# Optimization experiments

Measured on AMD Instinct MI355X. Metric: run time of the kernel, lower is better.

## Reference

```python
import jax, jax.numpy as jnp
import numpy as np

B, NP, K, E = 8, 4096, 1024, 262144   # graphs, nodes/graph, topk keep, edges
N = B * NP
EPS = 1e-5


def _glorot(k, fi, fo):
    lim = float(np.sqrt(6.0 / (fi + fo)))
    return jax.random.uniform(k, (fi, fo), jnp.float32, -lim, lim)


def setup_inputs() -> dict:
    key = jax.random.key(0)
    ks = jax.random.split(key, 16)
    pos = jax.random.normal(ks[0], (N, 3), jnp.float32)
    epg = E // B
    src = jax.random.randint(ks[1], (E,), 0, NP)
    dst = jax.random.randint(ks[2], (E,), 0, NP)
    off = jnp.repeat(jnp.arange(B) * NP, epg)   # edges stay within their graph
    edge_index = jnp.stack([src + off, dst + off]).astype(jnp.int32)
    batch = jnp.repeat(jnp.arange(B, dtype=jnp.int32), NP)
    inp = {"pos": pos, "edge_index": edge_index, "batch": batch,
           "p": jax.random.normal(ks[3], (3,), jnp.float32)}
    dims = [3, 64, 128, 128, 256, 512]
    for i in range(5):
        fi, fo = dims[i], dims[i + 1]
        inp[f"W{i+1}"] = _glorot(ks[4 + i], fi, fo)
        inp[f"b{i+1}"] = jnp.zeros((fo,), jnp.float32)
        inp[f"g{i+1}"] = jnp.ones((fo,), jnp.float32)
        inp[f"be{i+1}"] = jnp.zeros((fo,), jnp.float32)
    for i, (fi, fo) in enumerate([(512, 256), (256, 256), (256, 100)]):
        inp[f"fw{i+1}"] = _glorot(ks[9 + i], fi, fo)
        inp[f"fb{i+1}"] = jnp.zeros((fo,), jnp.float32)
    return inp


def _bn(x, g, b):
    # BatchNorm1d in training mode: batch stats over the node dim
    m = jnp.mean(x, 0)
    v = jnp.var(x, 0)
    return (x - m) * jax.lax.rsqrt(v + EPS) * g + b


def _gcn(x, src, dst, ew, W, bb, n):
    # GCNConv with add_self_loops=True, symmetric normalization.
    h = x @ W                                              # [n, out]
    deg = jax.ops.segment_sum(ew, dst, num_segments=n) + 1.0  # +1 self-loop
    dinv = jax.lax.rsqrt(deg)
    norm = dinv[src] * ew * dinv[dst]                      # masked edges -> 0
    agg = jax.ops.segment_sum(h[src] * norm[:, None], dst, num_segments=n)
    return agg + h * (dinv * dinv)[:, None] + bb           # self-loop term + bias


def _forward(pos, p, W1, b1, g1, be1, W2, b2, g2, be2, W3, b3, g3, be3,
             W4, b4, g4, be4, W5, b5, g5, be5, fw1, fb1, fw2, fb2, fw3, fb3,
             edge_index):
    # --- TopKPooling(ratio=1024): projection score, tanh, top-k per graph ---
    s = jnp.tanh(pos @ p / jnp.linalg.norm(p))             # [N]
    vals, idx = jax.lax.top_k(s.reshape(B, NP), K)         # [B,K]
    perm = (idx + (jnp.arange(B) * NP)[:, None]).reshape(-1)
    x = pos[perm] * vals.reshape(-1)[:, None]              # gate kept nodes
    Nn = B * K
    remap = jnp.full((N,), -1, jnp.int32).at[perm].set(jnp.arange(Nn, dtype=jnp.int32))
    src, dst = remap[edge_index[0]], remap[edge_index[1]]
    valid = (src >= 0) & (dst >= 0)
    ew = valid.astype(x.dtype)                             # 0-weight == removed edge
    src = jnp.where(valid, src, 0)
    dst = jnp.where(valid, dst, 0)
    for (W, bb, g, be) in ((W1, b1, g1, be1), (W2, b2, g2, be2),
                           (W3, b3, g3, be3), (W4, b4, g4, be4),
                           (W5, b5, g5, be5)):
        x = jax.nn.relu(_bn(_gcn(x, src, dst, ew, W, bb, Nn), g, be))
    # --- global sum pooling (torch_scatter default reduce='sum') ---
    batch_new = jnp.repeat(jnp.arange(B), K)
    x = jax.ops.segment_sum(x, batch_new, num_segments=B)  # [B,512]
    x = jax.nn.relu(x @ fw1 + fb1)
    x = jax.nn.relu(x @ fw2 + fb2)
    return jax.nn.log_softmax(x @ fw3 + fb3, axis=-1)      # [B,100]


def reference(pos, edge_index, batch, p, W1, b1, g1, be1, W2, b2, g2, be2,
              W3, b3, g3, be3, W4, b4, g4, be4, W5, b5, g5, be5,
              fw1, fb1, fw2, fb2, fw3, fb3):
    del batch  # graph ids are the fixed contiguous layout encoded in B, NP, K
    return _forward(pos, p, W1, b1, g1, be1, W2, b2, g2, be2, W3, b3, g3, be3,
                    W4, b4, g4, be4, W5, b5, g5, be5,
                    fw1, fb1, fw2, fb2, fw3, fb3, edge_index)
```

## Files before the change

### kernel.cpp

```cpp
#include <hip/hip_runtime.h>
#include <math.h>

#define NTOT 32768
#define NPG  4096
#define BGR  8
#define KK   1024
#define NN   8192
#define NE   262144

typedef __attribute__((ext_vector_type(8))) short bf16x8;
typedef __attribute__((ext_vector_type(4))) float f32x4;

static __device__ __forceinline__ unsigned short f2bf(float f) {
    unsigned u = __float_as_uint(f);
    return (unsigned short)((u + 0x7fffu + ((u >> 16) & 1u)) >> 16);
}
static __device__ __forceinline__ float bf2f(unsigned short b) {
    return __uint_as_float(((unsigned)b) << 16);
}

__global__ void k_init(int* remap, int* deg, int* cursor) {
    int i = blockIdx.x * blockDim.x + threadIdx.x;
    if (i < NTOT) remap[i] = -1;
    if (i < NN) { deg[i] = 0; cursor[i] = 0; }
}

__global__ __launch_bounds__(1024) void k_topk2(const float* __restrict__ pos,
                                                const float* __restrict__ p,
                                                int* __restrict__ remap,
                                                float* __restrict__ x0f,
                                                unsigned short* __restrict__ Ab0) {
    __shared__ unsigned skey[NPG];
    __shared__ float sval[NPG];
    __shared__ int hist[256];
    __shared__ int Sarr[256];
    __shared__ int wsum[16];
    __shared__ int s_bin, s_above;

    const int g = blockIdx.x, tid = threadIdx.x;
    const int lane = tid & 63, wid = tid >> 6;
    const float p0 = p[0], p1 = p[1], p2 = p[2];
    const float invn = 1.0f / sqrtf(p0 * p0 + p1 * p1 + p2 * p2);

    for (int i = tid; i < NPG; i += 1024) {
        const float* pp = pos + (size_t)(g * NPG + i) * 3;
        float s = tanhf((pp[0] * p0 + pp[1] * p1 + pp[2] * p2) * invn);
        sval[i] = s;
        unsigned b = __float_as_uint(s);
        skey[i] = (b & 0x80000000u) ? ~b : (b | 0x80000000u);
    }
    __syncthreads();

    unsigned prefix = 0;
    int needed = KK;
    for (int r = 0; r < 4; ++r) {
        const int sh = 24 - 8 * r;
        if (tid < 256) hist[tid] = 0;
        __syncthreads();
        for (int i = tid; i < NPG; i += 1024) {
            unsigned k = skey[i];
            bool act = (r == 0) || ((k >> (sh + 8)) == prefix);
            if (act) atomicAdd(&hist[(k >> sh) & 255u], 1);
        }
        __syncthreads();
        if (wid == 0) {
            int h0 = hist[4 * lane + 0], h1 = hist[4 * lane + 1];
            int h2 = hist[4 * lane + 2], h3 = hist[4 * lane + 3];
            int l3 = h3, l2 = h2 + l3, l1 = h1 + l2, l0 = h0 + l1;
            int t = l0;
            for (int off = 1; off < 64; off <<= 1) {
                int n = __shfl_down(t, off, 64);
                if (lane + off < 64) t += n;
            }
            int hi = t - l0;
            Sarr[4 * lane + 0] = l0 + hi;
            Sarr[4 * lane + 1] = l1 + hi;
            Sarr[4 * lane + 2] = l2 + hi;
            Sarr[4 * lane + 3] = l3 + hi;
        }
        __syncthreads();
        if (tid < 256) {
            int Sb = Sarr[tid];
            int Sb1 = (tid < 255) ? Sarr[tid + 1] : 0;
            if (Sb >= needed && Sb1 < needed) { s_bin = tid; s_above = Sb1; }
        }
        __syncthreads();
        needed -= s_above;
        prefix = (prefix << 8) | (unsigned)s_bin;
        __syncthreads();
    }
    const unsigned Tkey = prefix;
    const int needTies = needed;

    int tiebase = 0, keepbase = 0;
    for (int c = 0; c < 4; ++c) {
        const int i = c * 1024 + tid;
        const unsigned k = skey[i];
        const int tie = (k == Tkey) ? 1 : 0;
        int v = tie;
        for (int off = 1; off < 64; off <<= 1) {
            int n = __shfl_up(v, off, 64);
            if (lane >= off) v += n;
        }
        if (lane == 63) wsum[wid] = v;
        __syncthreads();
        if (wid == 0) {
            int w = (lane < 16) ? wsum[lane] : 0;
            for (int off = 1; off < 16; off <<= 1) {
                int n = __shfl_up(w, off, 64);
                if (lane >= off) w += n;
            }
            if (lane < 16) wsum[lane] = w;
        }
        __syncthreads();
        const int trank = tiebase + v + (wid > 0 ? wsum[wid - 1] : 0) - tie;
        const int ttot = wsum[15];
        const int keep = (k > Tkey) || (tie && trank < needTies);
        __syncthreads();
        int u = keep;
        for (int off = 1; off < 64; off <<= 1) {
            int n = __shfl_up(u, off, 64);
            if (lane >= off) u += n;
        }
        if (lane == 63) wsum[wid] = u;
        __syncthreads();
        if (wid == 0) {
            int w = (lane < 16) ? wsum[lane] : 0;
            for (int off = 1; off < 16; off <<= 1) {
                int n = __shfl_up(w, off, 64);
                if (lane >= off) w += n;
            }
            if (lane < 16) wsum[lane] = w;
        }
        __syncthreads();
        const int kincl = u + (wid > 0 ? wsum[wid - 1] : 0);
        const int ktot = wsum[15];
        if (keep) {
            int nn = g * KK + keepbase + kincl - 1;
            remap[g * NPG + i] = nn;
            float val = sval[i];
            const float* pp = pos + (size_t)(g * NPG + i) * 3;
            float v0 = pp[0] * val, v1 = pp[1] * val, v2 = pp[2] * val;
            x0f[(size_t)nn * 3 + 0] = v0;
            x0f[(size_t)nn * 3 + 1] = v1;
            x0f[(size_t)nn * 3 + 2] = v2;
            unsigned short* rw = Ab0 + (size_t)nn * 32;
            ushort4 a = make_ushort4(f2bf(v0), f2bf(v1), f2bf(v2), 0);
            ushort4 z = make_ushort4(0, 0, 0, 0);
            *(ushort4*)(rw) = a;
#pragma unroll
            for (int t = 1; t < 8; ++t) *(ushort4*)(rw + 4 * t) = z;
        }
        tiebase += ttot;
        keepbase += ktot;
        __syncthreads();
    }
}

__global__ void k_deg(const int* __restrict__ ei, const int* __restrict__ remap,
                      int* __restrict__ deg) {
    int e = blockIdx.x * blockDim.x + threadIdx.x;
    if (e >= NE) return;
    int s = remap[ei[e]];
    int d = remap[ei[NE + e]];
    if (s >= 0 && d >= 0) atomicAdd(&deg[d], 1);
}

__global__ __launch_bounds__(1024) void k_scan(const int* __restrict__ deg,
                                               int* __restrict__ rowptr) {
    __shared__ int part[1024];
    const int tid = threadIdx.x;
    const int base = tid * 8;
    int loc[8];
    int s = 0;
#pragma unroll
    for (int i = 0; i < 8; ++i) { loc[i] = s; s += deg[base + i]; }
    part[tid] = s;
    __syncthreads();
    for (int off = 1; off < 1024; off <<= 1) {
        int v = (tid >= off) ? part[tid - off] : 0;
        __syncthreads();
        part[tid] += v;
        __syncthreads();
    }
    int pre = (tid > 0) ? part[tid - 1] : 0;
#pragma unroll
    for (int i = 0; i < 8; ++i) rowptr[base + i] = pre + loc[i];
    if (tid == 1023) rowptr[NN] = pre + s;
}

__global__ void k_place2(const int* __restrict__ ei, const int* __restrict__ remap,
                         const int* __restrict__ deg, const int* __restrict__ rowptr,
                         int* __restrict__ cursor, int* __restrict__ col,
                         float* __restrict__ ew) {
    int e = blockIdx.x * blockDim.x + threadIdx.x;
    if (e >= NE) return;
    int s = remap[ei[e]];
    int d = remap[ei[NE + e]];
    if (s >= 0 && d >= 0) {
        int pos = rowptr[d] + atomicAdd(&cursor[d], 1);
        col[pos] = s;
        ew[pos] = rsqrtf((float)(deg[s] + 1)) * rsqrtf((float)(deg[d] + 1));
    }
}

__global__ void k_wt_all(const float* __restrict__ w0, const float* __restrict__ w1,
                         const float* __restrict__ w2, const float* __restrict__ w3,
                         const float* __restrict__ w4,
                         unsigned short* __restrict__ t0, unsigned short* __restrict__ t1,
                         unsigned short* __restrict__ t2, unsigned short* __restrict__ t3,
                         unsigned short* __restrict__ t4) {
    int i = blockIdx.x * blockDim.x + threadIdx.x;
    const float* W; unsigned short* T; int Kd, Nc, Kpad, base;
    if (i < 2048)        { W = w0; T = t0; Kd = 3;   Nc = 64;  Kpad = 32;  base = 0; }
    else if (i < 10240)  { W = w1; T = t1; Kd = 64;  Nc = 128; Kpad = 64;  base = 2048; }
    else if (i < 26624)  { W = w2; T = t2; Kd = 128; Nc = 128; Kpad = 128; base = 10240; }
    else if (i < 59392)  { W = w3; T = t3; Kd = 128; Nc = 256; Kpad = 128; base = 26624; }
    else if (i < 190464) { W = w4; T = t4; Kd = 256; Nc = 512; Kpad = 256; base = 59392; }
    else return;
    int j = i - base;
    int n = j / Kpad, k = j - n * Kpad;
    float v = (k < Kd) ? W[(size_t)k * Nc + n] : 0.0f;
    T[j] = f2bf(v);
}

__global__ __launch_bounds__(256) void k_mm2(const unsigned short* __restrict__ A,
                                             const unsigned short* __restrict__ WT,
                                             float* __restrict__ H,
                                             int Kd, int Nc) {
    const int lane = threadIdx.x & 63, wid = threadIdx.x >> 6;
    const int bm = blockIdx.x * 64 + (wid >> 1) * 32;
    const int bn = blockIdx.y * 64 + (wid & 1) * 32;
    const int fr = lane & 15;
    const int ko = (lane >> 4) << 3;
    const unsigned short* A0 = A + (size_t)(bm + fr) * Kd + ko;
    const unsigned short* B0 = WT + (size_t)(bn + fr) * Kd + ko;
    const size_t strA = (size_t)16 * Kd;
    f32x4 acc00 = {0,0,0,0}, acc01 = {0,0,0,0}, acc10 = {0,0,0,0}, acc11 = {0,0,0,0};
    for (int k0 = 0; k0 < Kd; k0 += 32) {
        bf16x8 a0 = *(const bf16x8*)(A0 + k0);
        bf16x8 a1 = *(const bf16x8*)(A0 + strA + k0);
        bf16x8 b0 = *(const bf16x8*)(B0 + k0);
        bf16x8 b1 = *(const bf16x8*)(B0 + strA + k0);
        acc00 = __builtin_amdgcn_mfma_f32_16x16x32_bf16(b0, a0, acc00, 0, 0, 0);
        acc01 = __builtin_amdgcn_mfma_f32_16x16x32_bf16(b1, a0, acc01, 0, 0, 0);
        acc10 = __builtin_amdgcn_mfma_f32_16x16x32_bf16(b0, a1, acc10, 0, 0, 0);
        acc11 = __builtin_amdgcn_mfma_f32_16x16x32_bf16(b1, a1, acc11, 0, 0, 0);
    }
    const int r = lane & 15;
    const int c4 = (lane >> 4) << 2;
#pragma unroll
    for (int tm = 0; tm < 2; ++tm) {
        const int row = bm + tm * 16 + r;
        const size_t basep = (size_t)row * Nc;
        const f32x4 aL = tm ? acc10 : acc00;
        const f32x4 aR = tm ? acc11 : acc01;
#pragma unroll
        for (int tn = 0; tn < 2; ++tn) {
            const f32x4 a = tn ? aR : aL;
            const int c = bn + tn * 16 + c4;
            *(float4*)&H[basep + c] = make_float4(a[0], a[1], a[2], a[3]);
        }
    }
}

#define BM 64
#define BNT 64
#define BKT 16
__global__ __launch_bounds__(256) void k_mm(const float* __restrict__ A,
                                            const float* __restrict__ W,
                                            float* __restrict__ H, int Kd, int Nc) {
    __shared__ float As[BM][BKT + 1];
    __shared__ float Bs[BKT][BNT + 1];
    const int bm = blockIdx.x * BM;
    const int bn = blockIdx.y * BNT;
    const int tid = threadIdx.x;
    const int tx = tid & 15, ty = tid >> 4;
    float acc[4][4] = {};
    for (int k0 = 0; k0 < Kd; k0 += BKT) {
        for (int t = 0; t < 4; ++t) {
            int i = tid + t * 256;
            int m = i >> 4, k = i & 15;
            As[m][k] = (k0 + k < Kd) ? A[(size_t)(bm + m) * Kd + k0 + k] : 0.0f;
        }
        for (int t = 0; t < 4; ++t) {
            int i = tid + t * 256;
            int k = i >> 6, n = i & 63;
            Bs[k][n] = (k0 + k < Kd) ? W[(size_t)(k0 + k) * Nc + bn + n] : 0.0f;
        }
        __syncthreads();
        for (int k = 0; k < BKT; ++k) {
            float a[4], b[4];
#pragma unroll
            for (int i = 0; i < 4; ++i) a[i] = As[ty * 4 + i][k];
#pragma unroll
            for (int j = 0; j < 4; ++j) b[j] = Bs[k][tx * 4 + j];
#pragma unroll
            for (int i = 0; i < 4; ++i)
#pragma unroll
                for (int j = 0; j < 4; ++j) acc[i][j] += a[i] * b[j];
        }
        __syncthreads();
    }
#pragma unroll
    for (int i = 0; i < 4; ++i)
        *(float4*)&H[(size_t)(bm + ty * 4 + i) * Nc + bn + tx * 4] =
            make_float4(acc[i][0], acc[i][1], acc[i][2], acc[i][3]);
}

#define BN1_ROWS 16
#define BN1_CHUNKS (NN / BN1_ROWS)
__global__ __launch_bounds__(256) void k_gfuse(const float* __restrict__ H,
                                               const int* __restrict__ rowptr,
                                               const int* __restrict__ col,
                                               const float* __restrict__ ew,
                                               const int* __restrict__ deg,
                                               const float* __restrict__ bias,
                                               float* __restrict__ Y,
                                               float* __restrict__ psum,
                                               float* __restrict__ psq, int Nc) {
    __shared__ float4 ls[256], lq[256];
    const int CHB = (Nc < 128) ? Nc : 128;
    const int CB = Nc / CHB;
    const int chunk = blockIdx.x / CB;
    const int cb = blockIdx.x - chunk * CB;
    const int QPB = CHB >> 2;
    const int tid = threadIdx.x;
    const int q = tid & (QPB - 1);
    const int rg = tid / QPB;
    const int NRG = 256 / QPB;
    const int RPT = BN1_ROWS / NRG;
    const int c = cb * CHB + (q << 2);
    const float4 b4 = *(const float4*)&bias[c];
    float4 s4 = make_float4(0, 0, 0, 0), q4 = make_float4(0, 0, 0, 0);
    for (int rr = 0; rr < RPT; ++rr) {
        const int n = chunk * BN1_ROWS + rg * RPT + rr;
        const int j0 = rowptr[n], j1 = rowptr[n + 1];
        const float inv = 1.0f / (float)(deg[n] + 1);
        float4 acc = *(const float4*)&H[(size_t)n * Nc + c];
        acc.x = acc.x * inv + b4.x;
        acc.y = acc.y * inv + b4.y;
        acc.z = acc.z * inv + b4.z;
        acc.w = acc.w * inv + b4.w;
        for (int j = j0; j < j1; ++j) {
            const float w = ew[j];
            const float4 hv = *(const float4*)&H[(size_t)col[j] * Nc + c];
            acc.x += hv.x * w; acc.y += hv.y * w; acc.z += hv.z * w; acc.w += hv.w * w;
        }
        *(float4*)&Y[(size_t)n * Nc + c] = acc;
        s4.x += acc.x; s4.y += acc.y; s4.z += acc.z; s4.w += acc.w;
        q4.x += acc.x * acc.x; q4.y += acc.y * acc.y;
        q4.z += acc.z * acc.z; q4.w += acc.w * acc.w;
    }
    ls[tid] = s4; lq[tid] = q4;
    __syncthreads();
    for (int st = 128; st >= QPB; st >>= 1) {
        if (tid < st) {
            float4 a = ls[tid], b = ls[tid + st];
            ls[tid] = make_float4(a.x + b.x, a.y + b.y, a.z + b.z, a.w + b.w);
            float4 e = lq[tid], f = lq[tid + st];
            lq[tid] = make_float4(e.x + f.x, e.y + f.y, e.z + f.z, e.w + f.w);
        }
        __syncthreads();
    }
    if (tid < QPB) {
        *(float4*)&psum[(size_t)chunk * Nc + c] = ls[tid];
        *(float4*)&psq[(size_t)chunk * Nc + c] = lq[tid];
    }
}

__global__ __launch_bounds__(256) void k_bn2p(const float* __restrict__ psum,
                                              const float* __restrict__ psq,
                                              const float* __restrict__ g,
                                              const float* __restrict__ be,
                                              float* __restrict__ scale,
                                              float* __restrict__ shift, int Nc) {
    __shared__ float ss[256], sq[256];
    const int c = blockIdx.x;
    const int t = threadIdx.x;
    float s = 0.0f, q = 0.0f;
    for (int b = t; b < BN1_CHUNKS; b += 256) {
        s += psum[(size_t)b * Nc + c];
        q += psq[(size_t)b * Nc + c];
    }
    ss[t] = s; sq[t] = q;
    __syncthreads();
    for (int st = 128; st > 0; st >>= 1) {
        if (t < st) { ss[t] += ss[t + st]; sq[t] += sq[t + st]; }
        __syncthreads();
    }
    if (t == 0) {
        double mean = (double)ss[0] / 8192.0;
        double var = (double)sq[0] / 8192.0 - mean * mean;
        float sc = (float)((double)g[c] / sqrt(var + 1e-5));
        scale[c] = sc;
        shift[c] = be[c] - (float)mean * sc;
    }
}

__global__ void k_bnapply2(const float* __restrict__ Y, const float* __restrict__ scale,
                           const float* __restrict__ shift, unsigned short* __restrict__ Ab,
                           int Nc) {
    int i = blockIdx.x * blockDim.x + threadIdx.x;
    int c4 = i & ((Nc >> 2) - 1);
    float4 v = ((const float4*)Y)[i];
    float4 sc = ((const float4*)scale)[c4];
    float4 sh = ((const float4*)shift)[c4];
    v.x = fmaxf(v.x * sc.x + sh.x, 0.0f);
    v.y = fmaxf(v.y * sc.y + sh.y, 0.0f);
    v.z = fmaxf(v.z * sc.z + sh.z, 0.0f);
    v.w = fmaxf(v.w * sc.w + sh.w, 0.0f);
    ((ushort4*)Ab)[i] = make_ushort4(f2bf(v.x), f2bf(v.y), f2bf(v.z), f2bf(v.w));
}

__global__ void k_bnapply(float* x, const float* __restrict__ scale,
                          const float* __restrict__ shift, int Nc) {
    int i = blockIdx.x * blockDim.x + threadIdx.x;
    int c4 = i & ((Nc >> 2) - 1);
    float4 v = ((const float4*)x)[i];
    float4 sc = ((const float4*)scale)[c4];
    float4 sh = ((const float4*)shift)[c4];
    v.x = fmaxf(v.x * sc.x + sh.x, 0.0f);
    v.y = fmaxf(v.y * sc.y + sh.y, 0.0f);
    v.z = fmaxf(v.z * sc.z + sh.z, 0.0f);
    v.w = fmaxf(v.w * sc.w + sh.w, 0.0f);
    ((float4*)x)[i] = v;
}

#define PR 32
__global__ __launch_bounds__(256) void k_pool_a(const unsigned short* __restrict__ x,
                                                float* __restrict__ part) {
    __shared__ float4 red[128];
    const int g = blockIdx.x >> 5;
    const int rs = blockIdx.x & 31;
    const int half = threadIdx.x >> 7;
    const int q = threadIdx.x & 127;
    const unsigned short* xp = x + (size_t)(g * KK + rs * PR + half * 16) * 512 + 4 * q;
    float4 s = make_float4(0, 0, 0, 0);
#pragma unroll
    for (int rr = 0; rr < 16; ++rr) {
        ushort4 v = *(const ushort4*)(xp + (size_t)rr * 512);
        s.x += bf2f(v.x); s.y += bf2f(v.y); s.z += bf2f(v.z); s.w += bf2f(v.w);
    }
    if (half == 1) red[q] = s;
    __syncthreads();
    if (half == 0) {
        float4 t = red[q];
        s.x += t.x; s.y += t.y; s.z += t.z; s.w += t.w;
        *(float4*)&part[(size_t)blockIdx.x * 512 + 4 * q] = s;
    }
}

__global__ __launch_bounds__(256) void k_pool(const float* __restrict__ x, float* pooled) {
    __shared__ float red[4][64];
    int g = blockIdx.x >> 3;
    int c0 = (blockIdx.x & 7) * 64;
    int c = threadIdx.x & 63;
    int rp = threadIdx.x >> 6;
    float s = 0;
    for (int r = rp; r < KK; r += 4)
        s += x[(size_t)(g * KK + r) * 512 + c0 + c];
    red[rp][c] = s;
    __syncthreads();
    if (rp == 0)
        pooled[g * 512 + c0 + c] = red[0][c] + red[1][c] + red[2][c] + red[3][c];
}

__global__ __launch_bounds__(256) void k_fc1(const float* __restrict__ part,
                                             const float* __restrict__ fw1,
                                             const float* __restrict__ fb1,
                                             float* __restrict__ t1, int nparts) {
    __shared__ float pooled[512];
    const int g = blockIdx.x, tid = threadIdx.x;
    for (int c = tid; c < 512; c += 256) {
        float s = 0;
        for (int i = 0; i < nparts; ++i) s += part[(size_t)(g * nparts + i) * 512 + c];
        pooled[c] = s;
    }
    __syncthreads();
    float acc = fb1[tid];
    for (int k = 0; k < 512; ++k) acc += pooled[k] * fw1[k * 256 + tid];
    t1[g * 256 + tid] = acc > 0.0f ? acc : 0.0f;
}

__global__ void k_fc(const float* __restrict__ in, const float* __restrict__ W,
                     const float* __restrict__ bias, float* out, int fi, int fo) {
    __shared__ float row[512];
    int g = blockIdx.x, tid = threadIdx.x;
    for (int k = tid; k < fi; k += blockDim.x) row[k] = in[g * fi + k];
    __syncthreads();
    if (tid < fo) {
        float acc = bias[tid];
        for (int k = 0; k < fi; ++k) acc += row[k] * W[k * fo + tid];
        out[g * fo + tid] = acc > 0.0f ? acc : 0.0f;
    }
}

__global__ __launch_bounds__(256) void k_fc23(const float* __restrict__ t1,
                                              const float* __restrict__ fw2,
                                              const float* __restrict__ fb2,
                                              const float* __restrict__ fw3,
                                              const float* __restrict__ fb3,
                                              float* __restrict__ out) {
    __shared__ float row[256];
    __shared__ float t2s[256];
    __shared__ float red[256];
    __shared__ float logits[100];
    const int g = blockIdx.x, tid = threadIdx.x;
    row[tid] = t1[g * 256 + tid];
    __syncthreads();
    float acc = fb2[tid];
    for (int k = 0; k < 256; ++k) acc += row[k] * fw2[k * 256 + tid];
    t2s[tid] = acc > 0.0f ? acc : 0.0f;
    __syncthreads();
    float v = -INFINITY;
    if (tid < 100) {
        float a3 = fb3[tid];
        for (int k = 0; k < 256; ++k) a3 += t2s[k] * fw3[k * 100 + tid];
        logits[tid] = a3;
        v = a3;
    }
    red[tid] = v;
    __syncthreads();
    for (int s = 128; s > 0; s >>= 1) {
        if (tid < s) red[tid] = fmaxf(red[tid], red[tid + s]);
        __syncthreads();
    }
    float mx = red[0];
    __syncthreads();
    red[tid] = (tid < 100) ? expf(logits[tid] - mx) : 0.0f;
    __syncthreads();
    for (int s = 128; s > 0; s >>= 1) {
        if (tid < s) red[tid] += red[tid + s];
        __syncthreads();
    }
    float lse = logf(red[0]);
    if (tid < 100) out[g * 100 + tid] = logits[tid] - mx - lse;
}

extern "C" void kernel_launch(void* const* d_in, const int* in_sizes, int n_in,
                              void* d_out, int out_size, void* d_ws, size_t ws_size,
                              hipStream_t stream) {
    const float* pos = (const float*)d_in[0];
    const int* ei = (const int*)d_in[1];
    const float* p = (const float*)d_in[3];
    const float *W[5], *bb[5], *gg[5], *be[5];
    for (int i = 0; i < 5; ++i) {
        W[i]  = (const float*)d_in[4 + 4 * i];
        bb[i] = (const float*)d_in[5 + 4 * i];
        gg[i] = (const float*)d_in[6 + 4 * i];
        be[i] = (const float*)d_in[7 + 4 * i];
    }
    const float* fw1 = (const float*)d_in[24]; const float* fb1 = (const float*)d_in[25];
    const float* fw2 = (const float*)d_in[26]; const float* fb2 = (const float*)d_in[27];
    const float* fw3 = (const float*)d_in[28]; const float* fb3 = (const float*)d_in[29];
    float* out = (float*)d_out;

    const int fins[5]  = {3, 64, 128, 128, 256};
    const int kpads[5] = {32, 64, 128, 128, 256};
    const int fouts[5] = {64, 128, 128, 256, 512};

    size_t off = 0;
    char* base = (char*)d_ws;
    auto alloc = [&](size_t bytes) { char* q = base + off; off += (bytes + 255) & ~(size_t)255; return q; };

    float* H      = (float*)alloc((size_t)NN * 512 * 4);
    float* Y      = (float*)alloc((size_t)NN * 512 * 4);
    int*   remap  = (int*)alloc((size_t)NTOT * 4);
    int*   deg    = (int*)alloc(NN * 4);
    int*   cursor = (int*)alloc(NN * 4);
    int*   rowptr = (int*)alloc((NN + 1) * 4);
    int*   ecol   = (int*)alloc((size_t)NE * 4);
    float* ew     = (float*)alloc((size_t)NE * 4);
    float* psum   = (float*)alloc((size_t)BN1_CHUNKS * 512 * 4);
    float* psq    = (float*)alloc((size_t)BN1_CHUNKS * 512 * 4);
    float* scale  = (float*)alloc(512 * 4);
    float* shift  = (float*)alloc(512 * 4);
    float* pooled = (float*)alloc(8 * 512 * 4);
    float* t1     = (float*)alloc(8 * 256 * 4);
    unsigned short* Ab0 = (unsigned short*)alloc((size_t)NN * 32 * 2);
    unsigned short* Ab  = (unsigned short*)alloc((size_t)NN * 512 * 2);
    float* part   = (float*)alloc((size_t)256 * 512 * 4);
    unsigned short* WT[5];
    for (int l = 0; l < 5; ++l) WT[l] = (unsigned short*)alloc((size_t)fouts[l] * kpads[l] * 2);
    const bool mfma = (ws_size >= off);

    k_init<<<NTOT / 256, 256, 0, stream>>>(remap, deg, cursor);
    k_topk2<<<BGR, 1024, 0, stream>>>(pos, p, remap, Y, Ab0);
    k_deg<<<NE / 256, 256, 0, stream>>>(ei, remap, deg);
    k_scan<<<1, 1024, 0, stream>>>(deg, rowptr);
    k_place2<<<NE / 256, 256, 0, stream>>>(ei, remap, deg, rowptr, cursor, ecol, ew);

    if (mfma) {
        k_wt_all<<<(190464 + 255) / 256, 256, 0, stream>>>(W[0], W[1], W[2], W[3], W[4],
                                                           WT[0], WT[1], WT[2], WT[3], WT[4]);
        for (int l = 0; l < 5; ++l) {
            int fo = fouts[l];
            const unsigned short* Ain = (l == 0) ? Ab0 : Ab;
            dim3 mg(NN / 64, fo / 64);
            k_mm2<<<mg, 256, 0, stream>>>(Ain, WT[l], H, kpads[l], fo);
            int cbs = (fo < 128) ? 1 : fo / 128;
            k_gfuse<<<BN1_CHUNKS * cbs, 256, 0, stream>>>(H, rowptr, ecol, ew, deg, bb[l],
                                                          Y, psum, psq, fo);
            k_bn2p<<<fo, 256, 0, stream>>>(psum, psq, gg[l], be[l], scale, shift, fo);
            k_bnapply2<<<(NN * fo) / 1024, 256, 0, stream>>>(Y, scale, shift, Ab, fo);
        }
        k_pool_a<<<256, 256, 0, stream>>>(Ab, part);
        k_fc1<<<8, 256, 0, stream>>>(part, fw1, fb1, t1, 32);
        k_fc23<<<8, 256, 0, stream>>>(t1, fw2, fb2, fw3, fb3, out);
    } else {
        for (int l = 0; l < 5; ++l) {
            int fi = fins[l], fo = fouts[l];
            dim3 mg(NN / BM, fo / BNT);
            k_mm<<<mg, 256, 0, stream>>>(Y, W[l], H, fi, fo);
            int cbs = (fo < 128) ? 1 : fo / 128;
            k_gfuse<<<BN1_CHUNKS * cbs, 256, 0, stream>>>(H, rowptr, ecol, ew, deg, bb[l],
                                                          Y, psum, psq, fo);
            k_bn2p<<<fo, 256, 0, stream>>>(psum, psq, gg[l], be[l], scale, shift, fo);
            k_bnapply<<<(NN * fo) / 1024, 256, 0, stream>>>(Y, scale, shift, fo);
        }
        k_pool<<<64, 256, 0, stream>>>(Y, pooled);
        k_fc<<<8, 256, 0, stream>>>(pooled, fw1, fb1, t1, 512, 256);
        k_fc23<<<8, 256, 0, stream>>>(t1, fw2, fb2, fw3, fb3, out);
    }
}
```

Measured before the change: 218.6 us.

## Fuse BN-apply into GEMM prologue and pooling, store GCN features as bf16

The separate BatchNorm-apply+ReLU+bf16 conversion kernel is removed. It is folded into the MFMA GEMM's A-operand load for layers 2-5 and into the final pooling kernel for layer 5. The GEMM output H is now written in bf16, and the gather/aggregation kernel reads bf16 rows, which halves the bytes of the irregular neighbour gathers. The trade-off is that the GEMM reads fp32 Y (twice the bytes of the old bf16 A) and redoes the affine transform once per column block, while aggregation precision drops to bf16 inputs.

Result: no change. 218.2 us (-0.2%).

```diff
diff --git a/kernel.cpp b/kernel.cpp
--- a/kernel.cpp
+++ b/kernel.cpp
@@ -224,22 +224,57 @@
     T[j] = f2bf(v);
 }
 
-__global__ __launch_bounds__(256) void k_mm2(const unsigned short* __restrict__ A,
+__global__ __launch_bounds__(256) void k_mm2(const unsigned short* __restrict__ Ab,
+                                             const float* __restrict__ Yin,
+                                             const float* __restrict__ scale,
+                                             const float* __restrict__ shift,
                                              const unsigned short* __restrict__ WT,
-                                             float* __restrict__ H,
+                                             unsigned short* __restrict__ Hb,
                                              int Kd, int Nc) {
     const int lane = threadIdx.x & 63, wid = threadIdx.x >> 6;
     const int bm = blockIdx.x * 64 + (wid >> 1) * 32;
     const int bn = blockIdx.y * 64 + (wid & 1) * 32;
     const int fr = lane & 15;
     const int ko = (lane >> 4) << 3;
-    const unsigned short* A0 = A + (size_t)(bm + fr) * Kd + ko;
+    const int row0 = bm + fr;
     const unsigned short* B0 = WT + (size_t)(bn + fr) * Kd + ko;
     const size_t strA = (size_t)16 * Kd;
     f32x4 acc00 = {0,0,0,0}, acc01 = {0,0,0,0}, acc10 = {0,0,0,0}, acc11 = {0,0,0,0};
     for (int k0 = 0; k0 < Kd; k0 += 32) {
-        bf16x8 a0 = *(const bf16x8*)(A0 + k0);
-        bf16x8 a1 = *(const bf16x8*)(A0 + strA + k0);
+        bf16x8 a0, a1;
+        if (Yin) {
+            const int cc = ko + k0;
+            const float4 sc0 = *(const float4*)&scale[cc];
+            const float4 sc1 = *(const float4*)&scale[cc + 4];
+            const float4 sh0 = *(const float4*)&shift[cc];
+            const float4 sh1 = *(const float4*)&shift[cc + 4];
+            const float* y0 = Yin + (size_t)row0 * Kd + cc;
+            const float* y1 = y0 + strA;
+#pragma unroll
+            for (int h = 0; h < 2; ++h) {
+                const float* yy = h ? y1 : y0;
+                float4 u = *(const float4*)yy;
+                float4 v = *(const float4*)(yy + 4);
+                float r0 = fmaxf(u.x * sc0.x + sh0.x, 0.0f);
+                float r1 = fmaxf(u.y * sc0.y + sh0.y, 0.0f);
+                float r2 = fmaxf(u.z * sc0.z + sh0.z, 0.0f);
+                float r3 = fmaxf(u.w * sc0.w + sh0.w, 0.0f);
+                float r4 = fmaxf(v.x * sc1.x + sh1.x, 0.0f);
+                float r5 = fmaxf(v.y * sc1.y + sh1.y, 0.0f);
+                float r6 = fmaxf(v.z * sc1.z + sh1.z, 0.0f);
+                float r7 = fmaxf(v.w * sc1.w + sh1.w, 0.0f);
+                bf16x8 a;
+                a[0] = (short)f2bf(r0); a[1] = (short)f2bf(r1);
+                a[2] = (short)f2bf(r2); a[3] = (short)f2bf(r3);
+                a[4] = (short)f2bf(r4); a[5] = (short)f2bf(r5);
+                a[6] = (short)f2bf(r6); a[7] = (short)f2bf(r7);
+                if (h) a1 = a; else a0 = a;
+            }
+        } else {
+            const unsigned short* A0 = Ab + (size_t)row0 * Kd + ko + k0;
+            a0 = *(const bf16x8*)A0;
+            a1 = *(const bf16x8*)(A0 + strA);
+        }
         bf16x8 b0 = *(const bf16x8*)(B0 + k0);
         bf16x8 b1 = *(const bf16x8*)(B0 + strA + k0);
         acc00 = __builtin_amdgcn_mfma_f32_16x16x32_bf16(b0, a0, acc00, 0, 0, 0);
@@ -259,7 +294,8 @@
         for (int tn = 0; tn < 2; ++tn) {
             const f32x4 a = tn ? aR : aL;
             const int c = bn + tn * 16 + c4;
-            *(float4*)&H[basep + c] = make_float4(a[0], a[1], a[2], a[3]);
+            *(ushort4*)&Hb[basep + c] = make_ushort4(f2bf(a[0]), f2bf(a[1]),
+                                                     f2bf(a[2]), f2bf(a[3]));
         }
     }
 }
@@ -310,7 +346,8 @@
 
 #define BN1_ROWS 16
 #define BN1_CHUNKS (NN / BN1_ROWS)
-__global__ __launch_bounds__(256) void k_gfuse(const float* __restrict__ H,
+__global__ __launch_bounds__(256) void k_gfuse(const unsigned short* __restrict__ Hb,
+                                               const float* __restrict__ Hf,
                                                const int* __restrict__ rowptr,
                                                const int* __restrict__ col,
                                                const float* __restrict__ ew,
@@ -337,15 +374,30 @@
         const int n = chunk * BN1_ROWS + rg * RPT + rr;
         const int j0 = rowptr[n], j1 = rowptr[n + 1];
         const float inv = 1.0f / (float)(deg[n] + 1);
-        float4 acc = *(const float4*)&H[(size_t)n * Nc + c];
+        float4 acc;
+        if (Hb) {
+            ushort4 hv = *(const ushort4*)&Hb[(size_t)n * Nc + c];
+            acc = make_float4(bf2f(hv.x), bf2f(hv.y), bf2f(hv.z), bf2f(hv.w));
+        } else {
+            acc = *(const float4*)&Hf[(size_t)n * Nc + c];
+        }
         acc.x = acc.x * inv + b4.x;
         acc.y = acc.y * inv + b4.y;
         acc.z = acc.z * inv + b4.z;
         acc.w = acc.w * inv + b4.w;
-        for (int j = j0; j < j1; ++j) {
-            const float w = ew[j];
-            const float4 hv = *(const float4*)&H[(size_t)col[j] * Nc + c];
-            acc.x += hv.x * w; acc.y += hv.y * w; acc.z += hv.z * w; acc.w += hv.w * w;
+        if (Hb) {
+            for (int j = j0; j < j1; ++j) {
+                const float w = ew[j];
+                ushort4 hv = *(const ushort4*)&Hb[(size_t)col[j] * Nc + c];
+                acc.x += bf2f(hv.x) * w; acc.y += bf2f(hv.y) * w;
+                acc.z += bf2f(hv.z) * w; acc.w += bf2f(hv.w) * w;
+            }
+        } else {
+            for (int j = j0; j < j1; ++j) {
+                const float w = ew[j];
+                const float4 hv = *(const float4*)&Hf[(size_t)col[j] * Nc + c];
+                acc.x += hv.x * w; acc.y += hv.y * w; acc.z += hv.z * w; acc.w += hv.w * w;
+            }
         }
         *(float4*)&Y[(size_t)n * Nc + c] = acc;
         s4.x += acc.x; s4.y += acc.y; s4.z += acc.z; s4.w += acc.w;
@@ -398,21 +450,6 @@
     }
 }
 
-__global__ void k_bnapply2(const float* __restrict__ Y, const float* __restrict__ scale,
-                           const float* __restrict__ shift, unsigned short* __restrict__ Ab,
-                           int Nc) {
-    int i = blockIdx.x * blockDim.x + threadIdx.x;
-    int c4 = i & ((Nc >> 2) - 1);
-    float4 v = ((const float4*)Y)[i];
-    float4 sc = ((const float4*)scale)[c4];
-    float4 sh = ((const float4*)shift)[c4];
-    v.x = fmaxf(v.x * sc.x + sh.x, 0.0f);
-    v.y = fmaxf(v.y * sc.y + sh.y, 0.0f);
-    v.z = fmaxf(v.z * sc.z + sh.z, 0.0f);
-    v.w = fmaxf(v.w * sc.w + sh.w, 0.0f);
-    ((ushort4*)Ab)[i] = make_ushort4(f2bf(v.x), f2bf(v.y), f2bf(v.z), f2bf(v.w));
-}
-
 __global__ void k_bnapply(float* x, const float* __restrict__ scale,
                           const float* __restrict__ shift, int Nc) {
     int i = blockIdx.x * blockDim.x + threadIdx.x;
@@ -428,19 +465,26 @@
 }
 
 #define PR 32
-__global__ __launch_bounds__(256) void k_pool_a(const unsigned short* __restrict__ x,
-                                                float* __restrict__ part) {
+__global__ __launch_bounds__(256) void k_pool_af(const float* __restrict__ Y,
+                                                 const float* __restrict__ scale,
+                                                 const float* __restrict__ shift,
+                                                 float* __restrict__ part) {
     __shared__ float4 red[128];
     const int g = blockIdx.x >> 5;
     const int rs = blockIdx.x & 31;
     const int half = threadIdx.x >> 7;
     const int q = threadIdx.x & 127;
-    const unsigned short* xp = x + (size_t)(g * KK + rs * PR + half * 16) * 512 + 4 * q;
+    const float4 sc = *(const float4*)&scale[4 * q];
+    const float4 sh = *(const float4*)&shift[4 * q];
+    const float* xp = Y + (size_t)(g * KK + rs * PR + half * 16) * 512 + 4 * q;
     float4 s = make_float4(0, 0, 0, 0);
 #pragma unroll
     for (int rr = 0; rr < 16; ++rr) {
-        ushort4 v = *(const ushort4*)(xp + (size_t)rr * 512);
-        s.x += bf2f(v.x); s.y += bf2f(v.y); s.z += bf2f(v.z); s.w += bf2f(v.w);
+        float4 v = *(const float4*)(xp + (size_t)rr * 512);
+        s.x += fmaxf(v.x * sc.x + sh.x, 0.0f);
+        s.y += fmaxf(v.y * sc.y + sh.y, 0.0f);
+        s.z += fmaxf(v.z * sc.z + sh.z, 0.0f);
+        s.w += fmaxf(v.w * sc.w + sh.w, 0.0f);
     }
     if (half == 1) red[q] = s;
     __syncthreads();
@@ -564,8 +608,8 @@
     char* base = (char*)d_ws;
     auto alloc = [&](size_t bytes) { char* q = base + off; off += (bytes + 255) & ~(size_t)255; return q; };
 
-    float* H      = (float*)alloc((size_t)NN * 512 * 4);
     float* Y      = (float*)alloc((size_t)NN * 512 * 4);
+    float* Hf     = (float*)alloc((size_t)NN * 512 * 4);
     int*   remap  = (int*)alloc((size_t)NTOT * 4);
     int*   deg    = (int*)alloc(NN * 4);
     int*   cursor = (int*)alloc(NN * 4);
@@ -579,10 +623,10 @@
     float* pooled = (float*)alloc(8 * 512 * 4);
     float* t1     = (float*)alloc(8 * 256 * 4);
     unsigned short* Ab0 = (unsigned short*)alloc((size_t)NN * 32 * 2);
-    unsigned short* Ab  = (unsigned short*)alloc((size_t)NN * 512 * 2);
     float* part   = (float*)alloc((size_t)256 * 512 * 4);
     unsigned short* WT[5];
     for (int l = 0; l < 5; ++l) WT[l] = (unsigned short*)alloc((size_t)fouts[l] * kpads[l] * 2);
+    unsigned short* Hb = (unsigned short*)Hf;
     const bool mfma = (ws_size >= off);
 
     k_init<<<NTOT / 256, 256, 0, stream>>>(remap, deg, cursor);
@@ -596,26 +640,29 @@
                                                            WT[0], WT[1], WT[2], WT[3], WT[4]);
         for (int l = 0; l < 5; ++l) {
             int fo = fouts[l];
-            const unsigned short* Ain = (l == 0) ? Ab0 : Ab;
             dim3 mg(NN / 64, fo / 64);
-            k_mm2<<<mg, 256, 0, stream>>>(Ain, WT[l], H, kpads[l], fo);
+            if (l == 0)
+                k_mm2<<<mg, 256, 0, stream>>>(Ab0, nullptr, nullptr, nullptr,
+                                              WT[l], Hb, kpads[l], fo);
+            else
+                k_mm2<<<mg, 256, 0, stream>>>(nullptr, Y, scale, shift,
+                                              WT[l], Hb, kpads[l], fo);
             int cbs = (fo < 128) ? 1 : fo / 128;
-            k_gfuse<<<BN1_CHUNKS * cbs, 256, 0, stream>>>(H, rowptr, ecol, ew, deg, bb[l],
-                                                          Y, psum, psq, fo);
+            k_gfuse<<<BN1_CHUNKS * cbs, 256, 0, stream>>>(Hb, nullptr, rowptr, ecol, ew,
+                                                          deg, bb[l], Y, psum, psq, fo);
             k_bn2p<<<fo, 256, 0, stream>>>(psum, psq, gg[l], be[l], scale, shift, fo);
-            k_bnapply2<<<(NN * fo) / 1024, 256, 0, stream>>>(Y, scale, shift, Ab, fo);
-        }
-        k_pool_a<<<256, 256, 0, stream>>>(Ab, part);
+        }
+        k_pool_af<<<256, 256, 0, stream>>>(Y, scale, shift, part);
         k_fc1<<<8, 256, 0, stream>>>(part, fw1, fb1, t1, 32);
         k_fc23<<<8, 256, 0, stream>>>(t1, fw2, fb2, fw3, fb3, out);
     } else {
         for (int l = 0; l < 5; ++l) {
             int fi = fins[l], fo = fouts[l];
             dim3 mg(NN / BM, fo / BNT);
-            k_mm<<<mg, 256, 0, stream>>>(Y, W[l], H, fi, fo);
+            k_mm<<<mg, 256, 0, stream>>>(Y, W[l], Hf, fi, fo);
             int cbs = (fo < 128) ? 1 : fo / 128;
-            k_gfuse<<<BN1_CHUNKS * cbs, 256, 0, stream>>>(H, rowptr, ecol, ew, deg, bb[l],
-                                                          Y, psum, psq, fo);
+            k_gfuse<<<BN1_CHUNKS * cbs, 256, 0, stream>>>(nullptr, Hf, rowptr, ecol, ew,
+                                                          deg, bb[l], Y, psum, psq, fo);
             k_bn2p<<<fo, 256, 0, stream>>>(psum, psq, gg[l], be[l], scale, shift, fo);
             k_bnapply<<<(NN * fo) / 1024, 256, 0, stream>>>(Y, scale, shift, fo);
         }
```
